# Kernel optimization log

Measured on AMD Instinct MI355X. Metric: run time of the kernel, lower is better.

## Reference

```python
import jax, jax.numpy as jnp
import numpy as np

KE_KCAL = 332.0637  # Coulomb constant in kcal/mol * Angstrom / e^2
R_CUT = 10.0
R_ON = R_CUT / 4.0
R_OFF = 3.0 * R_CUT / 4.0
MAX_Z = 86
FEAT_DIM = 128
N_ATOMS = 6144


def sigma(x):
    # torch.where(x > 0, exp(-1/x), 0) -- guard the exp arg so no NaN under jit
    xs = jnp.where(x > 0, x, 1.0)
    return jnp.where(x > 0, jnp.exp(-1.0 / xs), 0.0)


def f_switch(r):
    arg = (r - R_ON) / (R_OFF - R_ON)
    s_up = sigma(1.0 - arg)
    s_dn = sigma(arg)
    return s_up / (s_up + s_dn)


def setup_inputs() -> dict:
    key = jax.random.key(0)
    k_f, k_z, k_x, k_w, k_t = jax.random.split(key, 5)
    f = jax.random.normal(k_f, (N_ATOMS, FEAT_DIM), dtype=jnp.float32)
    z = jax.random.randint(k_z, (N_ATOMS,), 0, MAX_Z, dtype=jnp.int64)
    xyz = jax.random.uniform(k_x, (N_ATOMS, 3), dtype=jnp.float32) * 60.0  # ~60 A box
    total_charge = jnp.zeros((1,), dtype=jnp.float32)
    # learned params: Dense(feat_dim -> 1, no bias) and Embedding(max_z, 1) with padding row 0
    w_weight = jax.random.normal(k_w, (1, FEAT_DIM), dtype=jnp.float32) * 0.05
    z_table = jax.random.normal(k_t, (MAX_Z, 1), dtype=jnp.float32) * 0.05
    z_table = z_table.at[0].set(0.0)  # padding_idx=0
    return {"f": f, "z": z, "xyz": xyz, "total_charge": total_charge,
            "w_weight": w_weight, "z_table": z_table}


def reference(f, z, xyz, total_charge, w_weight, z_table):
    n = f.shape[0]
    # --- get_charge ---
    pred_charge = f @ w_weight.T + z_table[z]          # [N, 1]
    correction = (total_charge[0] - pred_charge.sum()) / n
    q = pred_charge + correction                       # [N, 1]
    qv = q[:, 0]                                       # [N]
    # --- get_en: pairwise distances via gram trick (no [N,N,3] intermediate) ---
    sq = jnp.sum(xyz * xyz, axis=-1)                   # [N]
    r2 = sq[:, None] + sq[None, :] - 2.0 * (xyz @ xyz.T)
    r2 = jnp.maximum(r2, 0.0)                          # [N, N]
    iu = jnp.triu(jnp.ones((n, n), dtype=bool), k=1)
    mask = iu & (r2 > 0.0)                             # j > i and r > 0, as in the torch code
    r2_safe = jnp.where(mask, r2, 1.0)
    r = jnp.sqrt(r2_safe)
    fs = f_switch(r)
    term = fs / jnp.sqrt(r2_safe + 1.0) + (1.0 - fs) / r
    pair_e = jnp.where(mask, qv[:, None] * qv[None, :] * term, 0.0)
    energy = KE_KCAL * jnp.sum(pair_e)
    return energy, q
```

## Files before the change

### kernel.cpp

```cpp
#include <hip/hip_runtime.h>

#define KE_KCAL 332.0637f

constexpr int N_ATOMS = 6144;
constexpr int NTI = 12;
constexpr int NTJ = 96;
constexpr int NREAL = 624;
constexpr int NQPART = 64;
constexpr int QSTRIDE = 32;

__global__ __launch_bounds__(256) void pred_kernel(
    const float* __restrict__ f, const int* __restrict__ z,
    const float* __restrict__ w, const float* __restrict__ ztab,
    const float* __restrict__ xyz,
    float* __restrict__ qpart, float4* __restrict__ xqp)
{
    int wid  = (blockIdx.x * blockDim.x + threadIdx.x) >> 6;
    int lane = threadIdx.x & 63;
    int base = wid * 4;
    if (base >= N_ATOMS) return;

    const float2* f2 = (const float2*)f;
    float2 wv = ((const float2*)w)[lane];

    float2 v0 = f2[(size_t)(base + 0) * 64 + lane];
    float2 v1 = f2[(size_t)(base + 1) * 64 + lane];
    float2 v2 = f2[(size_t)(base + 2) * 64 + lane];
    float2 v3 = f2[(size_t)(base + 3) * 64 + lane];

    float p0 = fmaf(v0.x, wv.x, v0.y * wv.y);
    float p1 = fmaf(v1.x, wv.x, v1.y * wv.y);
    float p2 = fmaf(v2.x, wv.x, v2.y * wv.y);
    float p3 = fmaf(v3.x, wv.x, v3.y * wv.y);

    #pragma unroll
    for (int off = 32; off > 0; off >>= 1) {
        p0 += __shfl_xor(p0, off, 64);
        p1 += __shfl_xor(p1, off, 64);
        p2 += __shfl_xor(p2, off, 64);
        p3 += __shfl_xor(p3, off, 64);
    }

    float ws_sum = 0.f;
    if (lane < 4) {
        int atom = base + lane;
        float pk = p0;
        pk = (lane == 1) ? p1 : pk;
        pk = (lane == 2) ? p2 : pk;
        pk = (lane == 3) ? p3 : pk;
        pk += ztab[z[atom]];
        xqp[atom] = make_float4(xyz[3*atom], xyz[3*atom+1], xyz[3*atom+2], pk);
        ws_sum = pk;
    }
    ws_sum += __shfl_xor(ws_sum, 1, 64);
    ws_sum += __shfl_xor(ws_sum, 2, 64);
    if (lane == 0)
        atomicAdd(&qpart[(wid & (NQPART - 1)) * QSTRIDE], ws_sum);
}

__global__ __launch_bounds__(256) void pair_kernel(
    const float4* __restrict__ xqp, const float* __restrict__ qpart,
    const float* __restrict__ total_charge,
    float* __restrict__ qout, float* __restrict__ epart,
    unsigned int* __restrict__ counter, float* __restrict__ out0)
{
    int bi = blockIdx.x, bj = blockIdx.y;
    if (bj < 8 * bi) return;
    int t = threadIdx.x;

    float s = 0.f;
    #pragma unroll
    for (int k = 0; k < NQPART; ++k) s += qpart[k * QSTRIDE];
    float corr = (total_charge[0] - s) * (1.0f / (float)N_ATOMS);

    __shared__ float4 sj[64];
    int gj0 = bj * 64;
    if (t < 64) {
        float4 a = xqp[gj0 + t];
        a.w += corr;
        sj[t] = a;
    }

    int i0 = bi * 512 + t, i1 = i0 + 256;
    float4 pi0 = xqp[i0], pi1 = xqp[i1];
    float q0 = pi0.w + corr, q1 = pi1.w + corr;
    if (bj == 8 * bi) { qout[i0] = q0; qout[i1] = q1; }
    __syncthreads();

    int jt0 = i0 - gj0, jt1 = i1 - gj0;
    float acc0 = 0.f, acc1 = 0.f;
    #pragma unroll 8
    for (int jj = 0; jj < 64; ++jj) {
        float4 pj = sj[jj];
        float dx0 = pi0.x - pj.x, dy0 = pi0.y - pj.y, dz0 = pi0.z - pj.z;
        float dx1 = pi1.x - pj.x, dy1 = pi1.y - pj.y, dz1 = pi1.z - pj.z;
        float r20 = fmaf(dx0, dx0, fmaf(dy0, dy0, dz0 * dz0));
        float r21 = fmaf(dx1, dx1, fmaf(dy1, dy1, dz1 * dz1));
        bool m0 = (jj > jt0) && (r20 > 0.f);
        bool m1 = (jj > jt1) && (r21 > 0.f);
        float r2s0 = m0 ? r20 : 1e8f;
        float r2s1 = m1 ? r21 : 1e8f;
        float qq0 = m0 ? q0 * pj.w : 0.f;
        float qq1 = m1 ? q1 * pj.w : 0.f;

        float t20 = __builtin_amdgcn_rsqf(r2s0);
        float t21 = __builtin_amdgcn_rsqf(r2s1);
        float u0 = fmaf(r2s0 * t20, 0.2f, -0.5f);
        float u1 = fmaf(r2s1 * t21, 0.2f, -0.5f);
        u0 = fminf(fmaxf(u0, 1e-3f), 0.999f);
        u1 = fminf(fmaxf(u1, 1e-3f), 0.999f);
        float d0 = (u0 + u0 - 1.f) * __builtin_amdgcn_rcpf(fmaf(-u0, u0, u0));
        float d1 = (u1 + u1 - 1.f) * __builtin_amdgcn_rcpf(fmaf(-u1, u1, u1));
        float fs0 = __builtin_amdgcn_rcpf(1.f + __expf(d0));
        float fs1 = __builtin_amdgcn_rcpf(1.f + __expf(d1));
        float t10 = __builtin_amdgcn_rsqf(r2s0 + 1.f);
        float t11 = __builtin_amdgcn_rsqf(r2s1 + 1.f);
        acc0 = fmaf(qq0, fmaf(fs0, t10 - t20, t20), acc0);
        acc1 = fmaf(qq1, fmaf(fs1, t11 - t21, t21), acc1);
    }
    float acc = acc0 + acc1;

    #pragma unroll
    for (int off = 32; off > 0; off >>= 1)
        acc += __shfl_down(acc, off, 64);
    __shared__ float wacc[4];
    if ((t & 63) == 0) wacc[t >> 6] = acc;
    __syncthreads();
    if (t == 0) {
        float be = wacc[0] + wacc[1] + wacc[2] + wacc[3];
        atomicAdd(&epart[((bi * 96 + bj) & 63)], be);
    }

    if (t < 64) {
        unsigned int old = 0;
        if (t == 0) {
            __threadfence();
            old = atomicAdd(counter, 1u);
        }
        old = __shfl(old, 0, 64);
        if (old == NREAL - 1) {
            float e = atomicAdd(&epart[t], 0.0f);
            #pragma unroll
            for (int off = 32; off > 0; off >>= 1)
                e += __shfl_down(e, off, 64);
            if (t == 0) out0[0] = KE_KCAL * e;
        }
    }
}

extern "C" void kernel_launch(void* const* d_in, const int* in_sizes, int n_in,
                              void* d_out, int out_size, void* d_ws, size_t ws_size,
                              hipStream_t stream) {
    const float* f    = (const float*)d_in[0];
    const int*   z    = (const int*)  d_in[1];
    const float* xyz  = (const float*)d_in[2];
    const float* qtot = (const float*)d_in[3];
    const float* w    = (const float*)d_in[4];
    const float* ztab = (const float*)d_in[5];
    float* out = (float*)d_out;

    char* wsb = (char*)d_ws;
    float*        epart   = (float*)(wsb + 0);
    unsigned int* counter = (unsigned int*)(wsb + 256);
    float*        qpart   = (float*)(wsb + 512);
    float4*       xqp     = (float4*)(wsb + 16384);

    hipMemsetAsync(d_ws, 0, 16384, stream);

    pred_kernel<<<N_ATOMS / 16, 256, 0, stream>>>(f, z, w, ztab, xyz,
                                                  qpart, xqp);
    dim3 grid(NTI, NTJ);
    pair_kernel<<<grid, 256, 0, stream>>>(xqp, qpart, qtot, out + 1, epart,
                                          counter, out);
}
```

Baseline: 99.51 us.

## Launch only upper-triangle pair tiles, drop memset, deterministic per-block charge partials

The pair kernel now uses a 1D grid of exactly the 1200 upper-triangle tiles (256 i-atoms by 64 j-atoms, one i per thread) rather than a 2D grid whose lower-triangle blocks exit early. The hipMemsetAsync is removed: block 0 of the pred kernel zeroes the energy partials and the counter, and each pred block writes its own charge partial without atomics. The pair kernel then reduces the 384 partials in parallel. This removes a launch, the empty blocks and the serial 64-load loop. In exchange, each tile index is decoded with a small while loop, and each thread does half the i-work, so there is less instruction-level parallelism per thread.

```diff
diff --git a/kernel.cpp b/kernel.cpp
--- a/kernel.cpp
+++ b/kernel.cpp
@@ -3,36 +3,36 @@
 #define KE_KCAL 332.0637f
 
 constexpr int N_ATOMS = 6144;
-constexpr int NTI = 12;
-constexpr int NTJ = 96;
-constexpr int NREAL = 624;
-constexpr int NQPART = 64;
-constexpr int QSTRIDE = 32;
+constexpr int NTI = 24;
+constexpr int NREAL = 1200;
+constexpr int NPRED = 384;
 
 __global__ __launch_bounds__(256) void pred_kernel(
     const float* __restrict__ f, const int* __restrict__ z,
     const float* __restrict__ w, const float* __restrict__ ztab,
     const float* __restrict__ xyz,
-    float* __restrict__ qpart, float4* __restrict__ xqp)
+    float* __restrict__ qpart, float4* __restrict__ xqp,
+    float* __restrict__ epart, unsigned int* __restrict__ counter)
 {
-    int wid  = (blockIdx.x * blockDim.x + threadIdx.x) >> 6;
-    int lane = threadIdx.x & 63;
-    int base = wid * 4;
-    if (base >= N_ATOMS) return;
+    int t = threadIdx.x, b = blockIdx.x;
+    int lane = t & 63, wid = t >> 6;
 
+    if (b == 0) {
+        if (t < 64) epart[t] = 0.f;
+        if (t == 64) *counter = 0u;
+    }
+
+    int base = b * 16 + wid * 4;
     const float2* f2 = (const float2*)f;
     float2 wv = ((const float2*)w)[lane];
-
     float2 v0 = f2[(size_t)(base + 0) * 64 + lane];
     float2 v1 = f2[(size_t)(base + 1) * 64 + lane];
     float2 v2 = f2[(size_t)(base + 2) * 64 + lane];
     float2 v3 = f2[(size_t)(base + 3) * 64 + lane];
-
     float p0 = fmaf(v0.x, wv.x, v0.y * wv.y);
     float p1 = fmaf(v1.x, wv.x, v1.y * wv.y);
     float p2 = fmaf(v2.x, wv.x, v2.y * wv.y);
     float p3 = fmaf(v3.x, wv.x, v3.y * wv.y);
-
     #pragma unroll
     for (int off = 32; off > 0; off >>= 1) {
         p0 += __shfl_xor(p0, off, 64);
@@ -40,7 +40,6 @@
         p2 += __shfl_xor(p2, off, 64);
         p3 += __shfl_xor(p3, off, 64);
     }
-
     float ws_sum = 0.f;
     if (lane < 4) {
         int atom = base + lane;
@@ -54,8 +53,11 @@
     }
     ws_sum += __shfl_xor(ws_sum, 1, 64);
     ws_sum += __shfl_xor(ws_sum, 2, 64);
-    if (lane == 0)
-        atomicAdd(&qpart[(wid & (NQPART - 1)) * QSTRIDE], ws_sum);
+
+    __shared__ float lred[4];
+    if (lane == 0) lred[wid] = ws_sum;
+    __syncthreads();
+    if (t == 0) qpart[b] = lred[0] + lred[1] + lred[2] + lred[3];
 }
 
 __global__ __launch_bounds__(256) void pair_kernel(
@@ -64,71 +66,65 @@
     float* __restrict__ qout, float* __restrict__ epart,
     unsigned int* __restrict__ counter, float* __restrict__ out0)
 {
-    int bi = blockIdx.x, bj = blockIdx.y;
-    if (bj < 8 * bi) return;
-    int t = threadIdx.x;
+    int t = threadIdx.x, b = blockIdx.x;
+    int lane = t & 63, wid = t >> 6;
+    __shared__ float lred[4];
+    __shared__ float4 sj[64];
 
-    float s = 0.f;
+    float s = qpart[t];
+    if (t < NPRED - 256) s += qpart[256 + t];
     #pragma unroll
-    for (int k = 0; k < NQPART; ++k) s += qpart[k * QSTRIDE];
-    float corr = (total_charge[0] - s) * (1.0f / (float)N_ATOMS);
+    for (int off = 32; off > 0; off >>= 1)
+        s += __shfl_xor(s, off, 64);
+    if (lane == 0) lred[wid] = s;
+    __syncthreads();
+    float S = lred[0] + lred[1] + lred[2] + lred[3];
+    float corr = (total_charge[0] - S) * (1.0f / (float)N_ATOMS);
 
-    __shared__ float4 sj[64];
+    int bi = 0, off = 0;
+    while (b >= off + (96 - 4 * bi)) { off += 96 - 4 * bi; ++bi; }
+    int bj = 4 * bi + (b - off);
+
     int gj0 = bj * 64;
     if (t < 64) {
         float4 a = xqp[gj0 + t];
         a.w += corr;
         sj[t] = a;
     }
-
-    int i0 = bi * 512 + t, i1 = i0 + 256;
-    float4 pi0 = xqp[i0], pi1 = xqp[i1];
-    float q0 = pi0.w + corr, q1 = pi1.w + corr;
-    if (bj == 8 * bi) { qout[i0] = q0; qout[i1] = q1; }
+    int gi = bi * 256 + t;
+    float4 pi = xqp[gi];
+    float qi = pi.w + corr;
+    if (bj == 4 * bi) qout[gi] = qi;
     __syncthreads();
 
-    int jt0 = i0 - gj0, jt1 = i1 - gj0;
-    float acc0 = 0.f, acc1 = 0.f;
+    int jthresh = gi - gj0;
+    float acc = 0.f;
     #pragma unroll 8
     for (int jj = 0; jj < 64; ++jj) {
         float4 pj = sj[jj];
-        float dx0 = pi0.x - pj.x, dy0 = pi0.y - pj.y, dz0 = pi0.z - pj.z;
-        float dx1 = pi1.x - pj.x, dy1 = pi1.y - pj.y, dz1 = pi1.z - pj.z;
-        float r20 = fmaf(dx0, dx0, fmaf(dy0, dy0, dz0 * dz0));
-        float r21 = fmaf(dx1, dx1, fmaf(dy1, dy1, dz1 * dz1));
-        bool m0 = (jj > jt0) && (r20 > 0.f);
-        bool m1 = (jj > jt1) && (r21 > 0.f);
-        float r2s0 = m0 ? r20 : 1e8f;
-        float r2s1 = m1 ? r21 : 1e8f;
-        float qq0 = m0 ? q0 * pj.w : 0.f;
-        float qq1 = m1 ? q1 * pj.w : 0.f;
-
-        float t20 = __builtin_amdgcn_rsqf(r2s0);
-        float t21 = __builtin_amdgcn_rsqf(r2s1);
-        float u0 = fmaf(r2s0 * t20, 0.2f, -0.5f);
-        float u1 = fmaf(r2s1 * t21, 0.2f, -0.5f);
-        u0 = fminf(fmaxf(u0, 1e-3f), 0.999f);
-        u1 = fminf(fmaxf(u1, 1e-3f), 0.999f);
-        float d0 = (u0 + u0 - 1.f) * __builtin_amdgcn_rcpf(fmaf(-u0, u0, u0));
-        float d1 = (u1 + u1 - 1.f) * __builtin_amdgcn_rcpf(fmaf(-u1, u1, u1));
-        float fs0 = __builtin_amdgcn_rcpf(1.f + __expf(d0));
-        float fs1 = __builtin_amdgcn_rcpf(1.f + __expf(d1));
-        float t10 = __builtin_amdgcn_rsqf(r2s0 + 1.f);
-        float t11 = __builtin_amdgcn_rsqf(r2s1 + 1.f);
-        acc0 = fmaf(qq0, fmaf(fs0, t10 - t20, t20), acc0);
-        acc1 = fmaf(qq1, fmaf(fs1, t11 - t21, t21), acc1);
+        float dx = pi.x - pj.x, dy = pi.y - pj.y, dz = pi.z - pj.z;
+        float r2 = fmaf(dx, dx, fmaf(dy, dy, dz * dz));
+        bool m = (jj > jthresh) && (r2 > 0.f);
+        float r2s = m ? r2 : 1e8f;
+        float qq  = m ? qi * pj.w : 0.f;
+        float t2  = __builtin_amdgcn_rsqf(r2s);
+        float u   = fmaf(r2s * t2, 0.2f, -0.5f);
+        u = fminf(fmaxf(u, 1e-3f), 0.999f);
+        float d   = (u + u - 1.f) * __builtin_amdgcn_rcpf(fmaf(-u, u, u));
+        float fs  = __builtin_amdgcn_rcpf(1.f + __expf(d));
+        float t1  = __builtin_amdgcn_rsqf(r2s + 1.f);
+        acc = fmaf(qq, fmaf(fs, t1 - t2, t2), acc);
     }
-    float acc = acc0 + acc1;
 
     #pragma unroll
-    for (int off = 32; off > 0; off >>= 1)
-        acc += __shfl_down(acc, off, 64);
-    __shared__ float wacc[4];
-    if ((t & 63) == 0) wacc[t >> 6] = acc;
+    for (int o2 = 32; o2 > 0; o2 >>= 1)
+        acc += __shfl_down(acc, o2, 64);
+    __syncthreads();
+    if (lane == 0) lred[wid] = acc;
     __syncthreads();
     if (t == 0) {
-        float be = wacc[0] + wacc[1] + wacc[2] + wacc[3];
-        atomicAdd(&epart[((bi * 96 + bj) & 63)], be);
+        float be = lred[0] + lred[1] + lred[2] + lred[3];
+        atomicAdd(&epart[b & 63], be);
     }
 
     if (t < 64) {
@@ -141,8 +137,8 @@
         if (old == NREAL - 1) {
             float e = atomicAdd(&epart[t], 0.0f);
             #pragma unroll
-            for (int off = 32; off > 0; off >>= 1)
-                e += __shfl_down(e, off, 64);
+            for (int o2 = 32; o2 > 0; o2 >>= 1)
+                e += __shfl_down(e, o2, 64);
             if (t == 0) out0[0] = KE_KCAL * e;
         }
     }
@@ -165,11 +161,8 @@
     float*        qpart   = (float*)(wsb + 512);
     float4*       xqp     = (float4*)(wsb + 16384);
 
-    hipMemsetAsync(d_ws, 0, 16384, stream);
-
-    pred_kernel<<<N_ATOMS / 16, 256, 0, stream>>>(f, z, w, ztab, xyz,
-                                                  qpart, xqp);
-    dim3 grid(NTI, NTJ);
-    pair_kernel<<<grid, 256, 0, stream>>>(xqp, qpart, qtot, out + 1, epart,
-                                          counter, out);
+    pred_kernel<<<NPRED, 256, 0, stream>>>(f, z, w, ztab, xyz,
+                                           qpart, xqp, epart, counter);
+    pair_kernel<<<NREAL, 256, 0, stream>>>(xqp, qpart, qtot, out + 1, epart,
+                                           counter, out);
 }
```

Result: faster. 94.39 us (-5.1%).
